# Performance work log

Hardware: AMD Instinct MI355X
Metric: run time of the kernel (lower is better)

Reference implementation:

```python
import jax, jax.numpy as jnp
import numpy as np

B, T, D, DH, DFF = 4, 2048, 1024, 1024, 4096


def setup_inputs() -> dict:
    key = jax.random.key(0)
    ks = jax.random.split(key, 8)
    s = 0.02
    return {
        "x": jax.random.normal(ks[0], (B, T, D), jnp.float32),
        "ln1_g": jnp.ones((D,), jnp.float32),
        "ln1_b": jnp.zeros((D,), jnp.float32),
        "W_q": jax.random.normal(ks[1], (D, DH), jnp.float32) * s,
        "b_q": jnp.zeros((DH,), jnp.float32),
        "W_k": jax.random.normal(ks[2], (D, DH), jnp.float32) * s,
        "b_k": jnp.zeros((DH,), jnp.float32),
        "W_v": jax.random.normal(ks[3], (D, DH), jnp.float32) * s,
        "b_v": jnp.zeros((DH,), jnp.float32),
        "ln2_g": jnp.ones((D,), jnp.float32),
        "ln2_b": jnp.zeros((D,), jnp.float32),
        "W_in": jax.random.normal(ks[4], (D, DFF), jnp.float32) * s,
        "b_in": jnp.zeros((DFF,), jnp.float32),
        "W_out": jax.random.normal(ks[5], (DFF, D), jnp.float32) * s,
        "b_out": jnp.zeros((D,), jnp.float32),
    }


def _layernorm(x, g, b, eps=1e-5):
    mu = jnp.mean(x, axis=-1, keepdims=True)
    var = jnp.var(x, axis=-1, keepdims=True)
    return (x - mu) * jax.lax.rsqrt(var + eps) * g + b


def reference(x, ln1_g, ln1_b, W_q, b_q, W_k, b_k, W_v, b_v,
              ln2_g, ln2_b, W_in, b_in, W_out, b_out):
    # --- attention branch (pre-LN) ---
    h = _layernorm(x, ln1_g, ln1_b)                      # [B,T,D]
    Q = h @ W_q + b_q                                    # [B,T,DH]
    K = h @ W_k + b_k
    V = h @ W_v + b_v
    scale = 1.0 / jnp.sqrt(jnp.asarray(K.shape[-1], h.dtype))
    att = jnp.einsum("btd,bsd->bts", Q, K) * scale       # [B,T,T]
    # NOTE: source calls att.masked_fill(...) without assignment -> mask
    # is discarded; faithfully no causal mask applied here.
    att = jax.nn.softmax(att, axis=-1)
    attn_out = jnp.einsum("bts,bsd->btd", att, V)        # [B,T,DH]
    x = x + attn_out
    # --- MLP branch (pre-LN) ---
    h2 = _layernorm(x, ln2_g, ln2_b)
    ff = jax.nn.gelu(h2 @ W_in + b_in, approximate=False)
    x = x + (ff @ W_out + b_out)
    return x
```

## Files before the change

### kernel.cpp

```cpp
#include <hip/hip_runtime.h>
#include <hip/hip_bf16.h>

#define B_    4
#define T_    2048
#define D_    1024
#define DH_   1024
#define DFF_  4096
#define MTOT  (B_ * T_)

using f32x4  = __attribute__((ext_vector_type(4))) float;
using bf16x8 = __attribute__((ext_vector_type(8))) short;

__device__ __forceinline__ unsigned short f2bf(float f) {
    unsigned u = __builtin_bit_cast(unsigned, f);
    u += 0x7fffu + ((u >> 16) & 1u);
    return (unsigned short)(u >> 16);
}

__device__ __forceinline__ void gload16(const short* g, short* l) {
    __builtin_amdgcn_global_load_lds(
        (const __attribute__((address_space(1))) unsigned int*)g,
        (__attribute__((address_space(3))) unsigned int*)l, 16, 0, 0);
}

__global__ __launch_bounds__(256) void transp_f32_bf16(
    const float* __restrict__ src, short* __restrict__ dst, int K, int N) {
    __shared__ float tile[32][33];
    int tk = blockIdx.y * 32, tn = blockIdx.x * 32;
    int tx = threadIdx.x & 31, ty = threadIdx.x >> 5;
#pragma unroll
    for (int i = 0; i < 4; i++) {
        int r = ty + i * 8;
        tile[r][tx] = src[(size_t)(tk + r) * N + tn + tx];
    }
    __syncthreads();
#pragma unroll
    for (int i = 0; i < 4; i++) {
        int r = ty + i * 8;
        dst[(size_t)(tn + r) * K + tk + tx] = f2bf(tile[tx][r]);
    }
}

__global__ void copyv(const float* __restrict__ s, float* __restrict__ d, int n) {
    int i = blockIdx.x * blockDim.x + threadIdx.x;
    if (i < n) d[i] = s[i];
}

__global__ __launch_bounds__(256) void ln_rows(
    const float* __restrict__ x, const float* __restrict__ g,
    const float* __restrict__ bta, short* __restrict__ out) {
    int row = blockIdx.x;
    const float* xr = x + (size_t)row * D_;
    int t = threadIdx.x;
    float4 v = *(const float4*)(xr + t * 4);
    float s  = v.x + v.y + v.z + v.w;
    float s2 = v.x * v.x + v.y * v.y + v.z * v.z + v.w * v.w;
#pragma unroll
    for (int off = 1; off < 64; off <<= 1) {
        s  += __shfl_xor(s, off);
        s2 += __shfl_xor(s2, off);
    }
    __shared__ float as_[4], as2_[4];
    int wave = t >> 6, lane = t & 63;
    if (lane == 0) { as_[wave] = s; as2_[wave] = s2; }
    __syncthreads();
    s  = as_[0] + as_[1] + as_[2] + as_[3];
    s2 = as2_[0] + as2_[1] + as2_[2] + as2_[3];
    float mean = s * (1.0f / D_);
    float var  = s2 * (1.0f / D_) - mean * mean;
    float rstd = rsqrtf(var + 1e-5f);
    float4 gv = *(const float4*)(g + t * 4);
    float4 bv = *(const float4*)(bta + t * 4);
    short4 o;
    o.x = f2bf((v.x - mean) * rstd * gv.x + bv.x);
    o.y = f2bf((v.y - mean) * rstd * gv.y + bv.y);
    o.z = f2bf((v.z - mean) * rstd * gv.z + bv.z);
    o.w = f2bf((v.w - mean) * rstd * gv.w + bv.w);
    *(short4*)(out + (size_t)row * D_ + t * 4) = o;
}

__global__ __launch_bounds__(256) void softmax_rows(float* __restrict__ S) {
    size_t row = blockIdx.x;
    float* sr = S + row * (size_t)T_;
    int t = threadIdx.x;
    float4 v0 = *(const float4*)(sr + t * 4);
    float4 v1 = *(const float4*)(sr + 1024 + t * 4);
    const float c = 0.03125f;
    float vv[8] = {v0.x * c, v0.y * c, v0.z * c, v0.w * c,
                   v1.x * c, v1.y * c, v1.z * c, v1.w * c};
    float mx = -1e30f;
#pragma unroll
    for (int i = 0; i < 8; i++) mx = fmaxf(mx, vv[i]);
#pragma unroll
    for (int off = 1; off < 64; off <<= 1) mx = fmaxf(mx, __shfl_xor(mx, off));
    __shared__ float sm_[4], ss[4];
    int wave = t >> 6, lane = t & 63;
    if (lane == 0) sm_[wave] = mx;
    __syncthreads();
    mx = fmaxf(fmaxf(sm_[0], sm_[1]), fmaxf(sm_[2], sm_[3]));
    float sum = 0.f;
#pragma unroll
    for (int i = 0; i < 8; i++) { vv[i] = expf(vv[i] - mx); sum += vv[i]; }
#pragma unroll
    for (int off = 1; off < 64; off <<= 1) sum += __shfl_xor(sum, off);
    if (lane == 0) ss[wave] = sum;
    __syncthreads();
    sum = ss[0] + ss[1] + ss[2] + ss[3];
    float inv = 1.0f / sum;
    short* pr = (short*)sr;
    short4 oa, ob;
    oa.x = f2bf(vv[0] * inv); oa.y = f2bf(vv[1] * inv);
    oa.z = f2bf(vv[2] * inv); oa.w = f2bf(vv[3] * inv);
    ob.x = f2bf(vv[4] * inv); ob.y = f2bf(vv[5] * inv);
    ob.z = f2bf(vv[6] * inv); ob.w = f2bf(vv[7] * inv);
    *(short4*)(pr + t * 4) = oa;
    *(short4*)(pr + 1024 + t * 4) = ob;
}

#define SLOT 8192
template<int BIAS_MODE, int ACT, int RES, int OUT_BF16>
__global__ __launch_bounds__(512, 2) void gemm8(
    const short* __restrict__ A, int lda, long long sA,
    const short* __restrict__ Bt, int ldb, long long sB,
    void* __restrict__ C, int ldc, long long sC,
    const float* __restrict__ bias,
    const float* __restrict__ res, int ldr, long long sR,
    int K) {
    extern __shared__ short smem_[];
    short* shA = smem_;
    short* shB = smem_ + 4 * SLOT;

    int gx = gridDim.x, gy = gridDim.y;
    int nwg = gx * gy * gridDim.z;
    int lid = blockIdx.x + gx * (blockIdx.y + gy * blockIdx.z);
    int q = nwg >> 3, r = nwg & 7, xcd = lid & 7, i_ = lid >> 3;
    int nid = (xcd < r ? xcd * (q + 1) : r * (q + 1) + (xcd - r) * q) + i_;
    int bx = nid % gx; int tmp_ = nid / gx; int by = tmp_ % gy; int z = tmp_ / gy;

    int bm = by * 256, bn = bx * 256;
    const short* gA = A  + (size_t)z * sA + (size_t)bm * lda;
    const short* gB = Bt + (size_t)z * sB + (size_t)bn * ldb;
    int tid = threadIdx.x, lane = tid & 63, w = tid >> 6;
    int wr = w >> 2, wc = w & 3;

    const short *pA0, *pA1, *pB0, *pB1;
    short *ldA0, *ldA1, *ldB0, *ldB1;
    {
        int o0 = tid * 16, o1 = (512 + tid) * 16;
        int s0 = o0 ^ (((o0 >> 7) & 3) << 4);
        int s1 = o1 ^ (((o1 >> 7) & 3) << 4);
        int r0 = s0 >> 6, c0 = (s0 & 63) >> 1;
        int r1 = s1 >> 6, c1 = (s1 & 63) >> 1;
        pA0 = gA + (size_t)r0 * lda + c0;
        pA1 = gA + (size_t)r1 * lda + c1;
        pB0 = gB + (size_t)r0 * ldb + c0;
        pB1 = gB + (size_t)r1 * ldb + c1;
        ldA0 = shA + tid * 8; ldA1 = shA + 4096 + tid * 8;
        ldB0 = shB + tid * 8; ldB1 = shB + 4096 + tid * 8;
    }
    int aoff[8], boff[4];
#pragma unroll
    for (int f = 0; f < 8; f++) {
        int b = (wr * 128 + f * 16 + (lane & 15)) * 64 + (lane >> 4) * 16;
        aoff[f] = b ^ (((b >> 7) & 3) << 4);
    }
#pragma unroll
    for (int f = 0; f < 4; f++) {
        int b = (wc * 64 + f * 16 + (lane & 15)) * 64 + (lane >> 4) * 16;
        boff[f] = b ^ (((b >> 7) & 3) << 4);
    }

    int nk = K >> 5;
    f32x4 acc[8][4] = {};

#pragma unroll
    for (int s = 0; s < 3; s++) {
        gload16(pA0 + s * 32, ldA0 + s * SLOT);  gload16(pA1 + s * 32, ldA1 + s * SLOT);
        gload16(pB0 + s * 32, ldB0 + s * SLOT);  gload16(pB1 + s * 32, ldB1 + s * SLOT);
    }
    asm volatile("s_waitcnt vmcnt(8)" ::: "memory");
    __builtin_amdgcn_s_barrier();

    for (int t = 0; t < nk; t++) {
        const char* sA_ = (const char*)(shA + (t & 3) * SLOT);
        const char* sB_ = (const char*)(shB + (t & 3) * SLOT);
        int e  = (t + 3) & 3;
        int ks = (t + 3 < nk ? t + 3 : nk - 1) * 32;
        bf16x8 a0 = *(const bf16x8*)(sA_ + aoff[0]);
        bf16x8 a1 = *(const bf16x8*)(sA_ + aoff[1]);
        bf16x8 a2 = *(const bf16x8*)(sA_ + aoff[2]);
        bf16x8 a3 = *(const bf16x8*)(sA_ + aoff[3]);
        bf16x8 b0 = *(const bf16x8*)(sB_ + boff[0]);
        bf16x8 b1 = *(const bf16x8*)(sB_ + boff[1]);
        bf16x8 b2 = *(const bf16x8*)(sB_ + boff[2]);
        bf16x8 b3 = *(const bf16x8*)(sB_ + boff[3]);
        gload16(pA0 + ks, shA + e * SLOT + tid * 8);
        gload16(pA1 + ks, shA + e * SLOT + 4096 + tid * 8);
        __builtin_amdgcn_s_barrier();
        asm volatile("s_waitcnt lgkmcnt(0)" ::: "memory");
        __builtin_amdgcn_sched_barrier(0);
        __builtin_amdgcn_s_setprio(1);
#define MF(r_, av) \
        acc[r_][0] = __builtin_amdgcn_mfma_f32_16x16x32_bf16(av, b0, acc[r_][0], 0, 0, 0); \
        acc[r_][1] = __builtin_amdgcn_mfma_f32_16x16x32_bf16(av, b1, acc[r_][1], 0, 0, 0); \
        acc[r_][2] = __builtin_amdgcn_mfma_f32_16x16x32_bf16(av, b2, acc[r_][2], 0, 0, 0); \
        acc[r_][3] = __builtin_amdgcn_mfma_f32_16x16x32_bf16(av, b3, acc[r_][3], 0, 0, 0);
        MF(0, a0) MF(1, a1) MF(2, a2) MF(3, a3)
        __builtin_amdgcn_s_setprio(0);
        __builtin_amdgcn_s_barrier();
        a0 = *(const bf16x8*)(sA_ + aoff[4]);
        a1 = *(const bf16x8*)(sA_ + aoff[5]);
        a2 = *(const bf16x8*)(sA_ + aoff[6]);
        a3 = *(const bf16x8*)(sA_ + aoff[7]);
        gload16(pB0 + ks, shB + e * SLOT + tid * 8);
        gload16(pB1 + ks, shB + e * SLOT + 4096 + tid * 8);
        asm volatile("s_waitcnt vmcnt(8)" ::: "memory");
        __builtin_amdgcn_s_barrier();
        asm volatile("s_waitcnt lgkmcnt(0)" ::: "memory");
        __builtin_amdgcn_sched_barrier(0);
        __builtin_amdgcn_s_setprio(1);
        MF(4, a0) MF(5, a1) MF(6, a2) MF(7, a3)
#undef MF
        __builtin_amdgcn_s_setprio(0);
        __builtin_amdgcn_s_barrier();
    }
    asm volatile("s_waitcnt vmcnt(0)" ::: "memory");

    size_t zc = (size_t)z * (size_t)sC;
#pragma unroll
    for (int fr = 0; fr < 8; fr++) {
#pragma unroll
        for (int fn = 0; fn < 4; fn++) {
            int col = bn + wc * 64 + fn * 16 + (lane & 15);
#pragma unroll
            for (int r_ = 0; r_ < 4; r_++) {
                int row = bm + wr * 128 + fr * 16 + (lane >> 4) * 4 + r_;
                float v = acc[fr][fn][r_];
                if (BIAS_MODE == 1) v += bias[col];
                else if (BIAS_MODE == 2) v += bias[row];
                if (ACT == 1) v = 0.5f * v * (1.0f + erff(v * 0.70710678118654752f));
                if (RES) v += res[(size_t)z * sR + (size_t)row * ldr + col];
                if (OUT_BF16) ((short*)C)[zc + (size_t)row * ldc + col] = f2bf(v);
                else          ((float*)C)[zc + (size_t)row * ldc + col] = v;
            }
        }
    }
}

#define SHBYTES (8 * SLOT * 2)

extern "C" void kernel_launch(void* const* d_in, const int* in_sizes, int n_in,
                              void* d_out, int out_size, void* d_ws, size_t ws_size,
                              hipStream_t stream) {
    const float* x    = (const float*)d_in[0];
    const float* ln1g = (const float*)d_in[1];
    const float* ln1b = (const float*)d_in[2];
    const float* Wq   = (const float*)d_in[3];
    const float* bq   = (const float*)d_in[4];
    const float* Wk   = (const float*)d_in[5];
    const float* bk   = (const float*)d_in[6];
    const float* Wv   = (const float*)d_in[7];
    const float* bv   = (const float*)d_in[8];
    const float* ln2g = (const float*)d_in[9];
    const float* ln2b = (const float*)d_in[10];
    const float* Win  = (const float*)d_in[11];
    const float* bin  = (const float*)d_in[12];
    const float* Wout = (const float*)d_in[13];
    const float* bout = (const float*)d_in[14];

    char* ws = (char*)d_ws;
    size_t off = 0;
    auto alloc = [&](size_t bytes) {
        void* p = ws + off;
        off += (bytes + 255) & ~(size_t)255;
        return p;
    };
    short* WqkT  = (short*)alloc((size_t)2048 * 1024 * 2);
    short* WvT   = (short*)alloc((size_t)1024 * 1024 * 2);
    short* WinT  = (short*)alloc((size_t)4096 * 1024 * 2);
    short* WoutT = (short*)alloc((size_t)1024 * 4096 * 2);
    float* bqk   = (float*)alloc((size_t)2048 * 4);
    short* h     = (short*)alloc((size_t)MTOT * 1024 * 2);
    short* QK    = (short*)alloc((size_t)MTOT * 2048 * 2);
    short* VT    = (short*)alloc((size_t)1024 * 8192 * 2);
    float* S     = (float*)alloc((size_t)4 * 2048 * 2048 * 4);
    float* x1    = (float*)alloc((size_t)MTOT * 1024 * 4);
    (void)ws_size; (void)in_sizes; (void)n_in; (void)out_size;

    hipFuncSetAttribute((const void*)gemm8<1,0,0,1>, hipFuncAttributeMaxDynamicSharedMemorySize, SHBYTES);
    hipFuncSetAttribute((const void*)gemm8<2,0,0,1>, hipFuncAttributeMaxDynamicSharedMemorySize, SHBYTES);
    hipFuncSetAttribute((const void*)gemm8<0,0,0,0>, hipFuncAttributeMaxDynamicSharedMemorySize, SHBYTES);
    hipFuncSetAttribute((const void*)gemm8<0,0,1,0>, hipFuncAttributeMaxDynamicSharedMemorySize, SHBYTES);
    hipFuncSetAttribute((const void*)gemm8<1,1,0,1>, hipFuncAttributeMaxDynamicSharedMemorySize, SHBYTES);
    hipFuncSetAttribute((const void*)gemm8<1,0,1,0>, hipFuncAttributeMaxDynamicSharedMemorySize, SHBYTES);

    transp_f32_bf16<<<dim3(32, 32), 256, 0, stream>>>(Wq, WqkT, 1024, 1024);
    transp_f32_bf16<<<dim3(32, 32), 256, 0, stream>>>(Wk, WqkT + (size_t)1024 * 1024, 1024, 1024);
    transp_f32_bf16<<<dim3(32, 32), 256, 0, stream>>>(Wv, WvT, 1024, 1024);
    transp_f32_bf16<<<dim3(128, 32), 256, 0, stream>>>(Win, WinT, 1024, 4096);
    transp_f32_bf16<<<dim3(32, 128), 256, 0, stream>>>(Wout, WoutT, 4096, 1024);
    copyv<<<4, 256, 0, stream>>>(bq, bqk, 1024);
    copyv<<<4, 256, 0, stream>>>(bk, bqk + 1024, 1024);

    ln_rows<<<MTOT, 256, 0, stream>>>(x, ln1g, ln1b, h);

    gemm8<1, 0, 0, 1><<<dim3(8, 32, 1), 512, SHBYTES, stream>>>(
        h, 1024, 0, WqkT, 1024, 0, QK, 2048, 0, bqk, nullptr, 0, 0, 1024);

    gemm8<2, 0, 0, 1><<<dim3(32, 4, 1), 512, SHBYTES, stream>>>(
        WvT, 1024, 0, h, 1024, 0, VT, 8192, 0, bv, nullptr, 0, 0, 1024);

    gemm8<0, 0, 0, 0><<<dim3(8, 8, 4), 512, SHBYTES, stream>>>(
        QK, 2048, 4194304LL, QK + 1024, 2048, 4194304LL,
        S, 2048, 4194304LL, nullptr, nullptr, 0, 0, 1024);

    softmax_rows<<<MTOT, 256, 0, stream>>>(S);

    gemm8<0, 0, 1, 0><<<dim3(4, 8, 4), 512, SHBYTES, stream>>>(
        (short*)S, 4096, 8388608LL, VT, 8192, 2048LL,
        x1, 1024, 2097152LL, nullptr, x, 1024, 2097152LL, 2048);

    ln_rows<<<MTOT, 256, 0, stream>>>(x1, ln2g, ln2b, h);

    short* ff = (short*)S;
    gemm8<1, 1, 0, 1><<<dim3(16, 32, 1), 512, SHBYTES, stream>>>(
        h, 1024, 0, WinT, 1024, 0, ff, 4096, 0, bin, nullptr, 0, 0, 1024);

    gemm8<1, 0, 1, 0><<<dim3(4, 32, 1), 512, SHBYTES, stream>>>(
        ff, 4096, 0, WoutT, 4096, 0, (float*)d_out, 1024, 0, bout,
        x1, 1024, 0, 4096);
}
```

Measured before the change: 454.9 us.

## Switch GEMM to BK=64 double-buffered LDS pipeline with strip-swizzled tile order

Restructures the bf16 GEMM main loop from a 4-stage ring of 32-wide K slices to a 2-stage double buffer of 64-wide K tiles, with a new XOR swizzle on 128-byte rows. Each iteration runs four MFMA phases with global loads interleaved between them. Workgroups are also remapped into 4-column strips to improve L2 reuse of B tiles. The goal is fewer barriers per K element and better cache locality, at the cost of shallower prefetch depth, which may expose more global memory latency.

```diff
diff --git a/kernel.cpp b/kernel.cpp
--- a/kernel.cpp
+++ b/kernel.cpp
@@ -117,7 +117,7 @@
     *(short4*)(pr + 1024 + t * 4) = ob;
 }
 
-#define SLOT 8192
+#define TILE_SH 16384
 template<int BIAS_MODE, int ACT, int RES, int OUT_BF16>
 __global__ __launch_bounds__(512, 2) void gemm8(
     const short* __restrict__ A, int lda, long long sA,
@@ -128,14 +128,18 @@
     int K) {
     extern __shared__ short smem_[];
     short* shA = smem_;
-    short* shB = smem_ + 4 * SLOT;
+    short* shB = smem_ + 2 * TILE_SH;
 
     int gx = gridDim.x, gy = gridDim.y;
-    int nwg = gx * gy * gridDim.z;
+    int n2d = gx * gy;
+    int nwg = n2d * gridDim.z;
     int lid = blockIdx.x + gx * (blockIdx.y + gy * blockIdx.z);
-    int q = nwg >> 3, r = nwg & 7, xcd = lid & 7, i_ = lid >> 3;
-    int nid = (xcd < r ? xcd * (q + 1) : r * (q + 1) + (xcd - r) * q) + i_;
-    int bx = nid % gx; int tmp_ = nid / gx; int by = tmp_ % gy; int z = tmp_ / gy;
+    int q = nwg >> 3, rq = nwg & 7, xcd = lid & 7, i_ = lid >> 3;
+    int nid = (xcd < rq ? xcd * (q + 1) : rq * (q + 1) + (xcd - rq) * q) + i_;
+    int z = nid / n2d, r2d = nid % n2d;
+    int sw = gy << 2;
+    int strip = r2d / sw, rr = r2d % sw;
+    int by = rr >> 2, bx = (strip << 2) + (rr & 3);
 
     int bm = by * 256, bn = bx * 256;
     const short* gA = A  + (size_t)z * sA + (size_t)bm * lda;
@@ -143,49 +147,51 @@
     int tid = threadIdx.x, lane = tid & 63, w = tid >> 6;
     int wr = w >> 2, wc = w & 3;
 
-    const short *pA0, *pA1, *pB0, *pB1;
-    short *ldA0, *ldA1, *ldB0, *ldB1;
-    {
-        int o0 = tid * 16, o1 = (512 + tid) * 16;
-        int s0 = o0 ^ (((o0 >> 7) & 3) << 4);
-        int s1 = o1 ^ (((o1 >> 7) & 3) << 4);
-        int r0 = s0 >> 6, c0 = (s0 & 63) >> 1;
-        int r1 = s1 >> 6, c1 = (s1 & 63) >> 1;
-        pA0 = gA + (size_t)r0 * lda + c0;
-        pA1 = gA + (size_t)r1 * lda + c1;
-        pB0 = gB + (size_t)r0 * ldb + c0;
-        pB1 = gB + (size_t)r1 * ldb + c1;
-        ldA0 = shA + tid * 8; ldA1 = shA + 4096 + tid * 8;
-        ldB0 = shB + tid * 8; ldB1 = shB + 4096 + tid * 8;
+    int rbase = tid >> 3;
+    int colb  = ((tid << 4) & 127) ^ ((rbase & 7) << 4);
+    int col   = colb >> 1;
+    const short* pA[4]; const short* pB[4];
+#pragma unroll
+    for (int c = 0; c < 4; c++) {
+        pA[c] = gA + (size_t)(c * 64 + rbase) * lda + col;
+        pB[c] = gB + (size_t)(c * 64 + rbase) * ldb + col;
     }
     int aoff[8], boff[4];
 #pragma unroll
     for (int f = 0; f < 8; f++) {
-        int b = (wr * 128 + f * 16 + (lane & 15)) * 64 + (lane >> 4) * 16;
-        aoff[f] = b ^ (((b >> 7) & 3) << 4);
+        int row = wr * 128 + f * 16 + (lane & 15);
+        aoff[f] = row * 128 + ((((lane >> 4) * 16)) ^ ((row & 7) << 4));
     }
 #pragma unroll
     for (int f = 0; f < 4; f++) {
-        int b = (wc * 64 + f * 16 + (lane & 15)) * 64 + (lane >> 4) * 16;
-        boff[f] = b ^ (((b >> 7) & 3) << 4);
-    }
-
-    int nk = K >> 5;
+        int row = wc * 64 + f * 16 + (lane & 15);
+        boff[f] = row * 128 + ((((lane >> 4) * 16)) ^ ((row & 7) << 4));
+    }
+
+    int nk = K >> 6;
     f32x4 acc[8][4] = {};
 
 #pragma unroll
-    for (int s = 0; s < 3; s++) {
-        gload16(pA0 + s * 32, ldA0 + s * SLOT);  gload16(pA1 + s * 32, ldA1 + s * SLOT);
-        gload16(pB0 + s * 32, ldB0 + s * SLOT);  gload16(pB1 + s * 32, ldB1 + s * SLOT);
-    }
-    asm volatile("s_waitcnt vmcnt(8)" ::: "memory");
+    for (int c = 0; c < 4; c++) {
+        gload16(pA[c], shA + c * 4096 + tid * 8);
+        gload16(pB[c], shB + c * 4096 + tid * 8);
+    }
+    asm volatile("s_waitcnt vmcnt(0)" ::: "memory");
     __builtin_amdgcn_s_barrier();
 
+#define MF(r_, av) \
+    acc[r_][0] = __builtin_amdgcn_mfma_f32_16x16x32_bf16(av, b0, acc[r_][0], 0, 0, 0); \
+    acc[r_][1] = __builtin_amdgcn_mfma_f32_16x16x32_bf16(av, b1, acc[r_][1], 0, 0, 0); \
+    acc[r_][2] = __builtin_amdgcn_mfma_f32_16x16x32_bf16(av, b2, acc[r_][2], 0, 0, 0); \
+    acc[r_][3] = __builtin_amdgcn_mfma_f32_16x16x32_bf16(av, b3, acc[r_][3], 0, 0, 0);
+
     for (int t = 0; t < nk; t++) {
-        const char* sA_ = (const char*)(shA + (t & 3) * SLOT);
-        const char* sB_ = (const char*)(shB + (t & 3) * SLOT);
-        int e  = (t + 3) & 3;
-        int ks = (t + 3 < nk ? t + 3 : nk - 1) * 32;
+        const char* sA_ = (const char*)(shA + (t & 1) * TILE_SH);
+        const char* sB_ = (const char*)(shB + (t & 1) * TILE_SH);
+        short* wA = shA + ((t + 1) & 1) * TILE_SH;
+        short* wB = shB + ((t + 1) & 1) * TILE_SH;
+        int ks = (t + 1 < nk ? t + 1 : nk - 1) << 6;
+
         bf16x8 a0 = *(const bf16x8*)(sA_ + aoff[0]);
         bf16x8 a1 = *(const bf16x8*)(sA_ + aoff[1]);
         bf16x8 a2 = *(const bf16x8*)(sA_ + aoff[2]);
@@ -194,36 +200,61 @@
         bf16x8 b1 = *(const bf16x8*)(sB_ + boff[1]);
         bf16x8 b2 = *(const bf16x8*)(sB_ + boff[2]);
         bf16x8 b3 = *(const bf16x8*)(sB_ + boff[3]);
-        gload16(pA0 + ks, shA + e * SLOT + tid * 8);
-        gload16(pA1 + ks, shA + e * SLOT + 4096 + tid * 8);
+        gload16(pA[0] + ks, wA + tid * 8);
+        gload16(pA[2] + ks, wA + 2 * 4096 + tid * 8);
         __builtin_amdgcn_s_barrier();
         asm volatile("s_waitcnt lgkmcnt(0)" ::: "memory");
-        __builtin_amdgcn_sched_barrier(0);
         __builtin_amdgcn_s_setprio(1);
-#define MF(r_, av) \
-        acc[r_][0] = __builtin_amdgcn_mfma_f32_16x16x32_bf16(av, b0, acc[r_][0], 0, 0, 0); \
-        acc[r_][1] = __builtin_amdgcn_mfma_f32_16x16x32_bf16(av, b1, acc[r_][1], 0, 0, 0); \
-        acc[r_][2] = __builtin_amdgcn_mfma_f32_16x16x32_bf16(av, b2, acc[r_][2], 0, 0, 0); \
-        acc[r_][3] = __builtin_amdgcn_mfma_f32_16x16x32_bf16(av, b3, acc[r_][3], 0, 0, 0);
         MF(0, a0) MF(1, a1) MF(2, a2) MF(3, a3)
         __builtin_amdgcn_s_setprio(0);
-        __builtin_amdgcn_s_barrier();
+        asm volatile("s_waitcnt vmcnt(2)" ::: "memory");
+        __builtin_amdgcn_s_barrier();
+
         a0 = *(const bf16x8*)(sA_ + aoff[4]);
         a1 = *(const bf16x8*)(sA_ + aoff[5]);
         a2 = *(const bf16x8*)(sA_ + aoff[6]);
         a3 = *(const bf16x8*)(sA_ + aoff[7]);
-        gload16(pB0 + ks, shB + e * SLOT + tid * 8);
-        gload16(pB1 + ks, shB + e * SLOT + 4096 + tid * 8);
-        asm volatile("s_waitcnt vmcnt(8)" ::: "memory");
+        gload16(pB[0] + ks, wB + tid * 8);
+        gload16(pB[1] + ks, wB + 4096 + tid * 8);
         __builtin_amdgcn_s_barrier();
         asm volatile("s_waitcnt lgkmcnt(0)" ::: "memory");
-        __builtin_amdgcn_sched_barrier(0);
         __builtin_amdgcn_s_setprio(1);
         MF(4, a0) MF(5, a1) MF(6, a2) MF(7, a3)
+        __builtin_amdgcn_s_setprio(0);
+        __builtin_amdgcn_s_barrier();
+
+        a0 = *(const bf16x8*)(sA_ + (aoff[0] ^ 64));
+        a1 = *(const bf16x8*)(sA_ + (aoff[1] ^ 64));
+        a2 = *(const bf16x8*)(sA_ + (aoff[2] ^ 64));
+        a3 = *(const bf16x8*)(sA_ + (aoff[3] ^ 64));
+        b0 = *(const bf16x8*)(sB_ + (boff[0] ^ 64));
+        b1 = *(const bf16x8*)(sB_ + (boff[1] ^ 64));
+        b2 = *(const bf16x8*)(sB_ + (boff[2] ^ 64));
+        b3 = *(const bf16x8*)(sB_ + (boff[3] ^ 64));
+        gload16(pB[2] + ks, wB + 2 * 4096 + tid * 8);
+        gload16(pB[3] + ks, wB + 3 * 4096 + tid * 8);
+        __builtin_amdgcn_s_barrier();
+        asm volatile("s_waitcnt lgkmcnt(0)" ::: "memory");
+        __builtin_amdgcn_s_setprio(1);
+        MF(0, a0) MF(1, a1) MF(2, a2) MF(3, a3)
+        __builtin_amdgcn_s_setprio(0);
+        __builtin_amdgcn_s_barrier();
+
+        a0 = *(const bf16x8*)(sA_ + (aoff[4] ^ 64));
+        a1 = *(const bf16x8*)(sA_ + (aoff[5] ^ 64));
+        a2 = *(const bf16x8*)(sA_ + (aoff[6] ^ 64));
+        a3 = *(const bf16x8*)(sA_ + (aoff[7] ^ 64));
+        gload16(pA[1] + ks, wA + 4096 + tid * 8);
+        gload16(pA[3] + ks, wA + 3 * 4096 + tid * 8);
+        __builtin_amdgcn_s_barrier();
+        asm volatile("s_waitcnt lgkmcnt(0)" ::: "memory");
+        __builtin_amdgcn_s_setprio(1);
+        MF(4, a0) MF(5, a1) MF(6, a2) MF(7, a3)
+        __builtin_amdgcn_s_setprio(0);
+        asm volatile("s_waitcnt vmcnt(2)" ::: "memory");
+        __builtin_amdgcn_s_barrier();
+    }
 #undef MF
-        __builtin_amdgcn_s_setprio(0);
-        __builtin_amdgcn_s_barrier();
-    }
     asm volatile("s_waitcnt vmcnt(0)" ::: "memory");
 
     size_t zc = (size_t)z * (size_t)sC;
@@ -231,23 +262,23 @@
     for (int fr = 0; fr < 8; fr++) {
 #pragma unroll
         for (int fn = 0; fn < 4; fn++) {
-            int col = bn + wc * 64 + fn * 16 + (lane & 15);
+            int colc = bn + wc * 64 + fn * 16 + (lane & 15);
 #pragma unroll
             for (int r_ = 0; r_ < 4; r_++) {
                 int row = bm + wr * 128 + fr * 16 + (lane >> 4) * 4 + r_;
                 float v = acc[fr][fn][r_];
-                if (BIAS_MODE == 1) v += bias[col];
+                if (BIAS_MODE == 1) v += bias[colc];
                 else if (BIAS_MODE == 2) v += bias[row];
                 if (ACT == 1) v = 0.5f * v * (1.0f + erff(v * 0.70710678118654752f));
-                if (RES) v += res[(size_t)z * sR + (size_t)row * ldr + col];
-                if (OUT_BF16) ((short*)C)[zc + (size_t)row * ldc + col] = f2bf(v);
-                else          ((float*)C)[zc + (size_t)row * ldc + col] = v;
+                if (RES) v += res[(size_t)z * sR + (size_t)row * ldr + colc];
+                if (OUT_BF16) ((short*)C)[zc + (size_t)row * ldc + colc] = f2bf(v);
+                else          ((float*)C)[zc + (size_t)row * ldc + colc] = v;
             }
         }
     }
 }
 
-#define SHBYTES (8 * SLOT * 2)
+#define SHBYTES (4 * TILE_SH * 2)
 
 extern "C" void kernel_launch(void* const* d_in, const int* in_sizes, int n_in,
                               void* d_out, int out_size, void* d_ws, size_t ws_size,
```

New measurement: 432.7 us. 4.9% less time.
